# Optimization experiments

Hardware: AMD Instinct MI355X
Metric: run time of the kernel (lower is better)

Reference implementation:

```python
import jax, jax.numpy as jnp
import numpy as np


def _compute_gradient(f, src, dst, egw):
    # f: [b, c, n] node features; src/dst: [b, e] edge endpoints; egw: [b, e, d]
    # gradient at node src = sum_edges pinvdx * (f[dst] - f[src])
    fT = f.transpose(0, 2, 1)  # b, n, c
    n = fT.shape[1]
    f_dst = jnp.take_along_axis(fT, dst[..., None], axis=1)  # b, e, c
    f_src = jnp.take_along_axis(fT, src[..., None], axis=1)  # b, e, c
    msg = egw[..., :, None] * (f_dst - f_src)[..., None, :]  # b, e, d, c
    b, e, d, c = msg.shape

    def seg(m, s):
        return jax.ops.segment_sum(m.reshape(e, d * c), s, num_segments=n)

    grad = jax.vmap(seg)(msg, src)  # b, n, d*c
    return grad.transpose(0, 2, 1)  # b, d*c, n


def _forward(x, t, nodes, node_weights, edge_gradient_weights, modes, sp_L,
             fc0_w, fc0_b, Wc, Ws, W0, ws_w, ws_b, gws_w, gws_b,
             fc1_w, fc1_b, fc2_w, fc2_b, directed_edges):
    D = nodes.shape[-1]
    # Fourier bases: modes [k,d,w] scaled by sp_L [d,w]
    temp = jnp.einsum('bxd,kdw->bxkw', nodes, modes * sp_L)
    bc, bs = jnp.cos(temp), jnp.sin(temp)
    b0 = jnp.ones(temp[:, :, :1, :].shape, temp.dtype)
    nw = node_weights[:, :, None, :]
    wbc, wbs, wb0 = bc * nw, bs * nw, b0 * nw

    x_value = x[:, :, :D]
    h = jnp.concatenate([x, t], -1) @ fc0_w + fc0_b  # b, n, c
    h = h.transpose(0, 2, 1)  # b, c, n

    src = directed_edges[..., 0]
    dst = directed_edges[..., 1]
    nlayers = ws_w.shape[0]
    for i in range(nlayers):
        # spectral convolution (real Fourier transform on scattered points)
        xc = jnp.einsum('bcx,bxkw->bckw', h, wbc)
        xs = -jnp.einsum('bcx,bxkw->bckw', h, wbs)
        x0 = jnp.einsum('bcx,bxkw->bckw', h, wb0)
        fc_ = jnp.einsum('bikw,iokw->bokw', xc, Wc[i]) - jnp.einsum('bikw,iokw->bokw', xs, Ws[i])
        fs_ = jnp.einsum('bikw,iokw->bokw', xs, Wc[i]) + jnp.einsum('bikw,iokw->bokw', xc, Ws[i])
        f0_ = jnp.einsum('bikw,iokw->bokw', x0, W0[i])
        x1 = (jnp.einsum('bokw,bxkw->box', f0_, b0)
              + 2.0 * jnp.einsum('bokw,bxkw->box', fc_, bc)
              - 2.0 * jnp.einsum('bokw,bxkw->box', fs_, bs))
        # pointwise linear (Conv1d kernel size 1)
        x2 = jnp.einsum('oc,bcx->box', ws_w[i], h) + ws_b[i][None, :, None]
        # gradient operator + softsign + Conv1d
        g = _compute_gradient(h, src, dst, edge_gradient_weights)  # b, d*c, n
        g = g / (1.0 + jnp.abs(g))  # softsign
        x3 = jnp.einsum('oc,bcx->box', gws_w[i], g) + gws_b[i][None, :, None]
        h = x1 + x2 + x3
        if i != nlayers - 1:
            h = jax.nn.gelu(h, approximate=False)

    h = h.transpose(0, 2, 1)  # b, n, c
    h = jax.nn.gelu(h @ fc1_w + fc1_b, approximate=False)
    h = h @ fc2_w + fc2_b
    return x_value + t * h


def setup_inputs() -> dict:
    B, N, E = 2, 20000, 100000
    D, W, K, C, L, FC, OUT = 3, 1, 128, 128, 3, 128, 3
    key = jax.random.key(0)
    k = jax.random.split(key, 16)
    x = jax.random.normal(k[0], (B, N, D), jnp.float32)
    t = jax.random.uniform(k[1], (B, N, 1), jnp.float32)
    node_mask = jnp.ones((B, N, 1), jnp.int32)
    nodes = jax.random.uniform(k[2], (B, N, D), jnp.float32)
    node_weights = jax.random.uniform(k[3], (B, N, W), jnp.float32) / N
    directed_edges = jax.random.randint(k[4], (B, E, 2), 0, N)
    edge_gradient_weights = jax.random.normal(k[5], (B, E, D), jnp.float32)
    modes = jax.random.normal(k[6], (K, D, W), jnp.float32) * (2.0 * np.pi)
    sp_L = jnp.ones((D, W), jnp.float32)
    fc0_w = jax.random.normal(k[7], (D + 1, C), jnp.float32) * 0.1
    fc0_b = jnp.zeros((C,), jnp.float32)
    scale = 1.0 / (C * C)
    Wc = jax.random.uniform(k[8], (L, C, C, K, W), jnp.float32) * scale
    Ws = jax.random.uniform(k[9], (L, C, C, K, W), jnp.float32) * scale
    W0 = jax.random.uniform(k[10], (L, C, C, 1, W), jnp.float32) * scale
    ws_w = jax.random.normal(k[11], (L, C, C), jnp.float32) * 0.05
    ws_b = jnp.zeros((L, C), jnp.float32)
    gws_w = jax.random.normal(k[12], (L, C, D * C), jnp.float32) * 0.05
    gws_b = jnp.zeros((L, C), jnp.float32)
    fc1_w = jax.random.normal(k[13], (C, FC), jnp.float32) * 0.05
    fc1_b = jnp.zeros((FC,), jnp.float32)
    fc2_w = jax.random.normal(k[14], (FC, OUT), jnp.float32) * 0.05
    fc2_b = jnp.zeros((OUT,), jnp.float32)
    return dict(x=x, t=t, node_mask=node_mask, nodes=nodes, node_weights=node_weights,
                directed_edges=directed_edges, edge_gradient_weights=edge_gradient_weights,
                modes=modes, sp_L=sp_L, fc0_w=fc0_w, fc0_b=fc0_b, Wc=Wc, Ws=Ws, W0=W0,
                ws_w=ws_w, ws_b=ws_b, gws_w=gws_w, gws_b=gws_b,
                fc1_w=fc1_w, fc1_b=fc1_b, fc2_w=fc2_w, fc2_b=fc2_b)


def reference(x, t, node_mask, nodes, node_weights, directed_edges, edge_gradient_weights,
              modes, sp_L, fc0_w, fc0_b, Wc, Ws, W0, ws_w, ws_b, gws_w, gws_b,
              fc1_w, fc1_b, fc2_w, fc2_b):
    del node_mask  # unpacked but unused in the original forward
    return _forward(x, t, nodes, node_weights, edge_gradient_weights, modes, sp_L,
                    fc0_w, fc0_b, Wc, Ws, W0, ws_w, ws_b, gws_w, gws_b,
                    fc1_w, fc1_b, fc2_w, fc2_b, directed_edges)
```

## Files before the change

kernel.cpp:

```cpp
#include <hip/hip_runtime.h>
#include <math.h>

#define BB 2
#define NN 20000
#define EE 100000
#define DD 3
#define KK 128
#define CC 128
#define LL 3
#define FCC 128
#define GJ (DD*CC)
#define KR 768
#define NP 20096
#define NCHK 157
#define G1CH 79
#define G1N 256

typedef __attribute__((ext_vector_type(8))) short bf16x8;
typedef __attribute__((ext_vector_type(4))) float f32x4;

__device__ inline unsigned short f2bf(float f) {
  unsigned int u = __float_as_uint(f);
  u += 0x7fffu + ((u >> 16) & 1u);
  return (unsigned short)(u >> 16);
}
__device__ inline float bf2f(unsigned short u) {
  return __uint_as_float(((unsigned int)u) << 16);
}

__device__ float d_nw[BB*NN];
__device__ __align__(16) unsigned short d_stackT[(size_t)BB*NP*KR];
__device__ __align__(16) unsigned short d_bcT[(size_t)BB*KK*NP];
__device__ __align__(16) unsigned short d_bsT[(size_t)BB*KK*NP];
__device__ __align__(16) unsigned short d_hTwT[(size_t)BB*CC*NP];
__device__ __align__(16) float d_hnewT[(size_t)BB*NP*CC];
__device__ __align__(16) float d_uT[(size_t)BB*NP*FCC];
__device__ __align__(16) unsigned short d_Amatb[BB*CC*KR];
__device__ __align__(16) unsigned short d_fc1wb[FCC*CC];
__device__ __align__(16) float d_part[(size_t)BB*G1CH*2*128*128];
__device__ float d_xc[BB*CC*KK];
__device__ float d_xs[BB*CC*KK];
__device__ float d_x0p[BB*NCHK*CC];
__device__ float d_fcv[BB*CC*KK];
__device__ float d_fsv[BB*CC*KK];
__device__ float d_bias[BB*CC];
__device__ int d_cnt[BB*NN];
__device__ int d_cursor[BB*NN];
__device__ int d_off[BB*(NN+1)];
__device__ __align__(16) float4 d_erec[(size_t)BB*EE];

__global__ __launch_bounds__(128) void k_basis(const float* __restrict__ nodes,
                                               const float* __restrict__ nodew,
                                               const float* __restrict__ modes,
                                               const float* __restrict__ spL) {
  int bn = blockIdx.x;
  int k  = threadIdx.x;
  int b = bn / NN, n = bn % NN;
  float x0 = nodes[bn*3+0], x1 = nodes[bn*3+1], x2 = nodes[bn*3+2];
  float tmp = x0*modes[k*3+0]*spL[0] + x1*modes[k*3+1]*spL[1] + x2*modes[k*3+2]*spL[2];
  float cv = cosf(tmp), sv = sinf(tmp);
  size_t row = (size_t)(b*NP + n);
  d_stackT[row*KR + k]       = f2bf(cv);
  d_stackT[row*KR + 128 + k] = f2bf(sv);
  if (k == 0) d_nw[bn] = nodew[bn];
}

__global__ __launch_bounds__(256) void k_basisT() {
  __shared__ unsigned short t1[32][136];
  __shared__ unsigned short t2[32][136];
  int blk = blockIdx.x;
  int nt = blk % 628, b = blk / 628;
  int n0 = nt*32;
  int tid = threadIdx.x;
  int kl = tid & 127, ng = tid >> 7;
  for (int nn = ng; nn < 32; nn += 2) {
    int n = n0 + nn;
    unsigned short cv = 0, sv = 0;
    if (n < NN) {
      const unsigned short* sp = d_stackT + ((size_t)(b*NP + n))*KR;
      cv = sp[kl]; sv = sp[128 + kl];
    }
    t1[nn][kl] = cv;
    t2[nn][kl] = sv;
  }
  __syncthreads();
  int nl = tid & 31, kg = tid >> 5;
  for (int k = kg; k < 128; k += 8) {
    d_bcT[((size_t)(b*KK + k))*NP + n0 + nl] = t1[nl][k];
    d_bsT[((size_t)(b*KK + k))*NP + n0 + nl] = t2[nl][k];
  }
}

__global__ __launch_bounds__(256) void k_csr_zero() {
  int tid = blockIdx.x*256 + threadIdx.x;
  if (tid < BB*NN) { d_cnt[tid] = 0; d_cursor[tid] = 0; }
}

__global__ __launch_bounds__(256) void k_csr_count(const int* __restrict__ edges) {
  int e = blockIdx.x*256 + threadIdx.x;
  if (e >= BB*EE) return;
  int b = e / EE;
  int src = edges[e*2 + 0];
  atomicAdd(&d_cnt[b*NN + src], 1);
}

__global__ __launch_bounds__(1024) void k_csr_scan() {
  int b = blockIdx.x;
  __shared__ int sdata[1024];
  __shared__ int carry_s;
  int tid = threadIdx.x;
  if (tid == 0) carry_s = 0;
  __syncthreads();
  for (int chunk = 0; chunk < 20; ++chunk) {
    int i = chunk*1024 + tid;
    int v = (i < NN) ? d_cnt[b*NN + i] : 0;
    sdata[tid] = v;
    __syncthreads();
    for (int s = 1; s < 1024; s <<= 1) {
      int tv = (tid >= s) ? sdata[tid - s] : 0;
      __syncthreads();
      sdata[tid] += tv;
      __syncthreads();
    }
    int excl = carry_s + sdata[tid] - v;
    if (i < NN) d_off[b*(NN+1) + i] = excl;
    __syncthreads();
    if (tid == 1023) carry_s += sdata[1023];
    __syncthreads();
  }
  if (tid == 0) d_off[b*(NN+1) + NN] = carry_s;
}

__global__ __launch_bounds__(256) void k_csr_scatter(const int* __restrict__ edges,
                                                     const float* __restrict__ egw) {
  int e = blockIdx.x*256 + threadIdx.x;
  if (e >= BB*EE) return;
  int b = e / EE;
  int src = edges[e*2 + 0];
  int dst = edges[e*2 + 1];
  int pos = atomicAdd(&d_cursor[b*NN + src], 1);
  d_erec[(size_t)b*EE + d_off[b*(NN+1) + src] + pos] =
      make_float4(__int_as_float(dst), egw[e*3+0], egw[e*3+1], egw[e*3+2]);
}

__global__ __launch_bounds__(256) void k_h0(const float* __restrict__ x,
                                            const float* __restrict__ t,
                                            const float* __restrict__ w,
                                            const float* __restrict__ bias) {
  int tid = blockIdx.x*256 + threadIdx.x;
  int c = tid & 127;
  int bn = tid >> 7;
  int b = bn / NN, n = bn % NN;
  const float* xv = x + bn*3;
  float acc = bias[c] + xv[0]*w[c] + xv[1]*w[CC+c] + xv[2]*w[2*CC+c]
            + t[bn]*w[3*CC+c];
  size_t row = (size_t)(b*NP + n);
  d_hnewT[row*CC + c] = acc;
  d_stackT[row*KR + 256 + c] = f2bf(acc);
}

__global__ __launch_bounds__(256) void k_hT0() {
  __shared__ unsigned short t[128][136];
  int chunk = blockIdx.x;
  int b = blockIdx.y;
  int n0 = chunk*128;
  int tid = threadIdx.x;
  int cl = tid & 127, ng = tid >> 7;
  for (int nn = ng; nn < 128; nn += 2) {
    int n = n0 + nn;
    unsigned short v = 0;
    if (n < NN) v = f2bf(d_hnewT[((size_t)(b*NP + n))*CC + cl] * d_nw[b*NN + n]);
    t[nn][cl] = v;
  }
  __syncthreads();
  int nl = tid & 31, cg = tid >> 5;
  for (int c = cg; c < 128; c += 8)
    for (int nn2 = 0; nn2 < 128; nn2 += 32)
      d_hTwT[((size_t)(b*CC + c))*NP + n0 + nn2 + nl] = t[nn2 + nl][c];
}

__global__ __launch_bounds__(256) void k_gemm1m() {
  __shared__ unsigned short Bsh[2][128][40];
  int chunk = blockIdx.x;
  int b = blockIdx.y;
  int tid = threadIdx.x, lane = tid & 63, wid = tid >> 6;
  int q = lane >> 4, m = lane & 15;
  f32x4 accC[2][8], accS[2][8];
  #pragma unroll
  for (int i = 0; i < 2; i++)
    #pragma unroll
    for (int j = 0; j < 8; j++) { accC[i][j] = (f32x4){0.f,0.f,0.f,0.f}; accS[i][j] = (f32x4){0.f,0.f,0.f,0.f}; }
  const unsigned short* Ab = d_hTwT + (size_t)b*CC*NP;
  const unsigned short* Bcp = d_bcT + (size_t)b*KK*NP;
  const unsigned short* Bsp = d_bsT + (size_t)b*KK*NP;
  int n0 = chunk*G1N;
  for (int s = 0; s < G1N/32; s++) {
    int nb = n0 + s*32;
    if (nb >= NP) break;
    __syncthreads();
    {
      int arr = tid >> 7, row = tid & 127;
      const unsigned short* src = (arr ? Bsp : Bcp) + (size_t)row*NP + nb;
      unsigned short* dr = &Bsh[arr][row][0];
      *(uint4*)&dr[0]  = *(const uint4*)&src[0];
      *(uint4*)&dr[8]  = *(const uint4*)&src[8];
      *(uint4*)&dr[16] = *(const uint4*)&src[16];
      *(uint4*)&dr[24] = *(const uint4*)&src[24];
    }
    __syncthreads();
    bf16x8 a0 = *(const bf16x8*)(Ab + (size_t)(wid*32 + m)*NP + nb + q*8);
    bf16x8 a1 = *(const bf16x8*)(Ab + (size_t)(wid*32 + 16 + m)*NP + nb + q*8);
    #pragma unroll
    for (int kt = 0; kt < 8; kt++) {
      bf16x8 bcf = *(const bf16x8*)&Bsh[0][kt*16 + m][q*8];
      bf16x8 bsf = *(const bf16x8*)&Bsh[1][kt*16 + m][q*8];
      accC[0][kt] = __builtin_amdgcn_mfma_f32_16x16x32_bf16(a0, bcf, accC[0][kt], 0, 0, 0);
      accC[1][kt] = __builtin_amdgcn_mfma_f32_16x16x32_bf16(a1, bcf, accC[1][kt], 0, 0, 0);
      accS[0][kt] = __builtin_amdgcn_mfma_f32_16x16x32_bf16(a0, bsf, accS[0][kt], 0, 0, 0);
      accS[1][kt] = __builtin_amdgcn_mfma_f32_16x16x32_bf16(a1, bsf, accS[1][kt], 0, 0, 0);
    }
  }
  float* base = d_part + (((size_t)b*G1CH + chunk)*2)*16384;
  #pragma unroll
  for (int mt = 0; mt < 2; mt++)
    #pragma unroll
    for (int kt = 0; kt < 8; kt++)
      #pragma unroll
      for (int r = 0; r < 4; r++) {
        int c = wid*32 + mt*16 + q*4 + r;
        int k = kt*16 + m;
        base[c*128 + k]         =  accC[mt][kt][r];
        base[16384 + c*128 + k] = -accS[mt][kt][r];
      }
}

__global__ __launch_bounds__(256) void k_reduce1() {
  int tid = blockIdx.x*256 + threadIdx.x;
  int k = tid & 127;
  int c = (tid >> 7) & 127;
  int arr = (tid >> 14) & 1;
  int b = tid >> 15;
  const float* p = d_part + (((size_t)b*G1CH)*2 + arr)*16384 + c*128 + k;
  float acc = 0.f;
  for (int ch = 0; ch < G1CH; ch++) acc += p[(size_t)ch*2*16384];
  if (arr == 0) d_xc[(b*CC + c)*KK + k] = acc;
  else          d_xs[(b*CC + c)*KK + k] = acc;
}

__global__ __launch_bounds__(256) void k_x0() {
  int chunk = blockIdx.x;
  int b = blockIdx.y;
  int tid = threadIdx.x;
  int c = tid >> 1, half = tid & 1;
  const unsigned short* p = d_hTwT + ((size_t)(b*CC + c))*NP + chunk*128 + half*64;
  float acc = 0.f;
  #pragma unroll
  for (int i = 0; i < 8; i++) {
    ushort4 v0 = *(const ushort4*)&p[i*8];
    ushort4 v1 = *(const ushort4*)&p[i*8 + 4];
    acc += bf2f(v0.x) + bf2f(v0.y) + bf2f(v0.z) + bf2f(v0.w)
         + bf2f(v1.x) + bf2f(v1.y) + bf2f(v1.z) + bf2f(v1.w);
  }
  __shared__ float red[128][2];
  red[c][half] = acc;
  __syncthreads();
  if (half == 0) d_x0p[(b*NCHK + chunk)*CC + c] = red[c][0] + red[c][1];
}

__global__ __launch_bounds__(128) void k_spec(const float* __restrict__ Wc,
                                              const float* __restrict__ Ws, int l) {
  int b = blockIdx.x >> 7;
  int o = blockIdx.x & 127;
  int k = threadIdx.x;
  const float* wcp = Wc + ((size_t)(l*CC)*CC + o)*KK + k;
  const float* wsp = Ws + ((size_t)(l*CC)*CC + o)*KK + k;
  float fc = 0.f, fs = 0.f;
  for (int i = 0; i < CC; i++) {
    float xcv = d_xc[(b*CC + i)*KK + k];
    float xsv = d_xs[(b*CC + i)*KK + k];
    float wcv = wcp[(size_t)i*CC*KK];
    float wsv = wsp[(size_t)i*CC*KK];
    fc += xcv*wcv - xsv*wsv;
    fs += xsv*wcv + xcv*wsv;
  }
  d_fcv[(b*CC + o)*KK + k] = fc;
  d_fsv[(b*CC + o)*KK + k] = fs;
}

__global__ __launch_bounds__(128) void k_f0(const float* __restrict__ W0,
                                            const float* __restrict__ wsb,
                                            const float* __restrict__ gwsb, int l) {
  int b = blockIdx.x;
  int o = threadIdx.x;
  __shared__ float sx[CC];
  float xv = 0.f;
  for (int p = 0; p < NCHK; p++) xv += d_x0p[(b*NCHK + p)*CC + o];
  sx[o] = xv;
  __syncthreads();
  float acc = 0.f;
  for (int i = 0; i < CC; i++) acc += sx[i]*W0[(l*CC + i)*CC + o];
  d_bias[b*CC + o] = acc + wsb[l*CC + o] + gwsb[l*CC + o];
}

__global__ __launch_bounds__(128) void k_buildAb(const float* __restrict__ wsw,
                                                 const float* __restrict__ gwsw, int l) {
  int bo = blockIdx.x;
  int b = bo >> 7, o = bo & 127;
  int t = threadIdx.x;
  unsigned short* dst = d_Amatb + (size_t)bo*KR;
  dst[t]       = f2bf( 2.f*d_fcv[(size_t)bo*KK + t]);
  dst[128 + t] = f2bf(-2.f*d_fsv[(size_t)bo*KK + t]);
  dst[256 + t] = f2bf(wsw[(l*CC + o)*CC + t]);
  #pragma unroll
  for (int j = 0; j < 3; j++)
    dst[384 + j*128 + t] = f2bf(gwsw[(size_t)(l*CC + o)*GJ + j*128 + t]);
}

__global__ __launch_bounds__(128) void k_fc1w(const float* __restrict__ fc1w) {
  int c = blockIdx.x;
  int o2 = threadIdx.x;
  d_fc1wb[o2*CC + c] = f2bf(fc1w[c*FCC + o2]);
}

__global__ __launch_bounds__(128) void k_grad_csr() {
  int bn = blockIdx.x;
  int b = bn / NN, n = bn % NN;
  int c = threadIdx.x;
  int beg = d_off[b*(NN+1) + n];
  int end = d_off[b*(NN+1) + n + 1];
  const float4* rp = d_erec + (size_t)b*EE;
  const float* hb = d_hnewT + (size_t)b*NP*CC + c;
  float a0 = 0.f, a1 = 0.f, a2 = 0.f;
  float sw0 = 0.f, sw1 = 0.f, sw2 = 0.f;
  int p = beg;
  for (; p + 2 <= end; p += 2) {
    float4 r1 = rp[p], r2 = rp[p+1];
    float f1 = hb[(size_t)__float_as_int(r1.x)*CC];
    float f2 = hb[(size_t)__float_as_int(r2.x)*CC];
    a0 += r1.y*f1 + r2.y*f2;
    a1 += r1.z*f1 + r2.z*f2;
    a2 += r1.w*f1 + r2.w*f2;
    sw0 += r1.y + r2.y; sw1 += r1.z + r2.z; sw2 += r1.w + r2.w;
  }
  if (p < end) {
    float4 r1 = rp[p];
    float f1 = hb[(size_t)__float_as_int(r1.x)*CC];
    a0 += r1.y*f1; a1 += r1.z*f1; a2 += r1.w*f1;
    sw0 += r1.y; sw1 += r1.z; sw2 += r1.w;
  }
  float fs = d_hnewT[((size_t)(b*NP + n))*CC + c];
  a0 -= sw0*fs; a1 -= sw1*fs; a2 -= sw2*fs;
  unsigned short* gp = d_stackT + ((size_t)(b*NP + n))*KR + 384;
  gp[c]        = f2bf(a0/(1.f + fabsf(a0)));
  gp[CC + c]   = f2bf(a1/(1.f + fabsf(a1)));
  gp[2*CC + c] = f2bf(a2/(1.f + fabsf(a2)));
}

__global__ __launch_bounds__(256) void k_mfma(int koff, int K,
                                              const unsigned short* __restrict__ W, size_t wstride,
                                              float* __restrict__ Out,
                                              const float* __restrict__ bias, int bias_stride,
                                              int gelu, int aux) {
  __shared__ unsigned short As[128*40];
  __shared__ unsigned short Bs[128*40];
  int b = blockIdx.z;
  int n_base = blockIdx.x*128;
  int tid = threadIdx.x;
  int lane = tid & 63, wid = tid >> 6;
  int q = lane >> 4, m = lane & 15;

  f32x4 acc[2][8];
  #pragma unroll
  for (int i = 0; i < 2; i++)
    #pragma unroll
    for (int j = 0; j < 8; j++) acc[i][j] = (f32x4){0.f,0.f,0.f,0.f};

  const unsigned short* Wb = W + (size_t)b*wstride;
  const unsigned short* Ab = d_stackT + (size_t)b*NP*KR + koff;

  for (int k0 = 0; k0 < K; k0 += 32) {
    __syncthreads();
    #pragma unroll
    for (int i = 0; i < 2; i++) {
      int row = (tid >> 2) + i*64;
      int e8  = (tid & 3)*8;
      *(uint4*)&As[row*40 + e8] = *(const uint4*)(Ab + (size_t)(n_base + row)*KR + k0 + e8);
      *(uint4*)&Bs[row*40 + e8] = *(const uint4*)(Wb + (size_t)row*K + k0 + e8);
    }
    __syncthreads();
    bf16x8 a0 = *(const bf16x8*)&As[(wid*32 + m)*40 + q*8];
    bf16x8 a1 = *(const bf16x8*)&As[(wid*32 + 16 + m)*40 + q*8];
    #pragma unroll
    for (int ot = 0; ot < 8; ot++) {
      bf16x8 bf = *(const bf16x8*)&Bs[(ot*16 + m)*40 + q*8];
      acc[0][ot] = __builtin_amdgcn_mfma_f32_16x16x32_bf16(a0, bf, acc[0][ot], 0, 0, 0);
      acc[1][ot] = __builtin_amdgcn_mfma_f32_16x16x32_bf16(a1, bf, acc[1][ot], 0, 0, 0);
    }
  }

  const float* bp = bias + (size_t)b*bias_stride;
  #pragma unroll
  for (int nt = 0; nt < 2; nt++) {
    int nb4 = n_base + wid*32 + nt*16 + q*4;
    float nw4[4];
    #pragma unroll
    for (int r = 0; r < 4; r++)
      nw4[r] = (aux && nb4 + r < NN) ? d_nw[b*NN + nb4 + r] : 0.f;
    #pragma unroll
    for (int ot = 0; ot < 8; ot++) {
      int o = ot*16 + m;
      float bvv = bp[o];
      float vals[4];
      #pragma unroll
      for (int r = 0; r < 4; r++) {
        float v = acc[nt][ot][r] + bvv;
        if (gelu) v = 0.5f*v*(1.f + erff(v*0.70710678118f));
        vals[r] = v;
        Out[((size_t)(b*NP + nb4 + r))*128 + o] = v;
        if (aux && nb4 + r < NN)
          d_stackT[((size_t)(b*NP + nb4 + r))*KR + 256 + o] = f2bf(v);
      }
      if (aux) {
        ushort4 pk;
        pk.x = f2bf(vals[0]*nw4[0]);
        pk.y = f2bf(vals[1]*nw4[1]);
        pk.z = f2bf(vals[2]*nw4[2]);
        pk.w = f2bf(vals[3]*nw4[3]);
        *(ushort4*)&d_hTwT[((size_t)(b*CC + o))*NP + nb4] = pk;
      }
    }
  }
}

__global__ __launch_bounds__(256) void k_out(const float* __restrict__ x,
                                             const float* __restrict__ t,
                                             const float* __restrict__ fc2w,
                                             const float* __restrict__ fc2b,
                                             float* __restrict__ out) {
  int tid = blockIdx.x*256 + threadIdx.x;
  if (tid >= BB*NN) return;
  int b = tid / NN, n = tid % NN;
  const float* up = d_uT + ((size_t)(b*NP + n))*FCC;
  float a0 = fc2b[0], a1 = fc2b[1], a2v = fc2b[2];
  #pragma unroll 4
  for (int o2 = 0; o2 < FCC; o2 += 4) {
    float4 uv = *(const float4*)&up[o2];
    a0  += uv.x*fc2w[(o2+0)*3+0] + uv.y*fc2w[(o2+1)*3+0] + uv.z*fc2w[(o2+2)*3+0] + uv.w*fc2w[(o2+3)*3+0];
    a1  += uv.x*fc2w[(o2+0)*3+1] + uv.y*fc2w[(o2+1)*3+1] + uv.z*fc2w[(o2+2)*3+1] + uv.w*fc2w[(o2+3)*3+1];
    a2v += uv.x*fc2w[(o2+0)*3+2] + uv.y*fc2w[(o2+1)*3+2] + uv.z*fc2w[(o2+2)*3+2] + uv.w*fc2w[(o2+3)*3+2];
  }
  float tv = t[tid];
  out[tid*3 + 0] = x[tid*3 + 0] + tv*a0;
  out[tid*3 + 1] = x[tid*3 + 1] + tv*a1;
  out[tid*3 + 2] = x[tid*3 + 2] + tv*a2v;
}

extern "C" void kernel_launch(void* const* d_in, const int* in_sizes, int n_in,
                              void* d_out, int out_size, void* d_ws, size_t ws_size,
                              hipStream_t stream) {
  const float* x     = (const float*)d_in[0];
  const float* t     = (const float*)d_in[1];
  const float* nodes = (const float*)d_in[3];
  const float* nodew = (const float*)d_in[4];
  const int*   edges = (const int*)d_in[5];
  const float* egw   = (const float*)d_in[6];
  const float* modes = (const float*)d_in[7];
  const float* spL   = (const float*)d_in[8];
  const float* fc0w  = (const float*)d_in[9];
  const float* fc0b  = (const float*)d_in[10];
  const float* Wc    = (const float*)d_in[11];
  const float* Ws    = (const float*)d_in[12];
  const float* W0    = (const float*)d_in[13];
  const float* wsw   = (const float*)d_in[14];
  const float* wsb   = (const float*)d_in[15];
  const float* gwsw  = (const float*)d_in[16];
  const float* gwsb  = (const float*)d_in[17];
  const float* fc1w  = (const float*)d_in[18];
  const float* fc1b  = (const float*)d_in[19];
  const float* fc2w  = (const float*)d_in[20];
  const float* fc2b  = (const float*)d_in[21];
  float* out = (float*)d_out;

  unsigned short* d_Amatb_p; hipGetSymbolAddress((void**)&d_Amatb_p, HIP_SYMBOL(d_Amatb));
  unsigned short* d_fc1wb_p; hipGetSymbolAddress((void**)&d_fc1wb_p, HIP_SYMBOL(d_fc1wb));
  float* d_hnewT_p; hipGetSymbolAddress((void**)&d_hnewT_p, HIP_SYMBOL(d_hnewT));
  float* d_uT_p;    hipGetSymbolAddress((void**)&d_uT_p,    HIP_SYMBOL(d_uT));
  float* d_bias_p;  hipGetSymbolAddress((void**)&d_bias_p,  HIP_SYMBOL(d_bias));

  hipLaunchKernelGGL(k_basis, dim3(BB*NN), dim3(128), 0, stream, nodes, nodew, modes, spL);
  hipLaunchKernelGGL(k_basisT, dim3(628*BB), dim3(256), 0, stream);
  hipLaunchKernelGGL(k_h0, dim3(BB*NN*CC/256), dim3(256), 0, stream, x, t, fc0w, fc0b);
  hipLaunchKernelGGL(k_hT0, dim3(NCHK, BB), dim3(256), 0, stream);
  hipLaunchKernelGGL(k_fc1w, dim3(CC), dim3(FCC), 0, stream, fc1w);
  hipLaunchKernelGGL(k_csr_zero, dim3((BB*NN + 255)/256), dim3(256), 0, stream);
  hipLaunchKernelGGL(k_csr_count, dim3((BB*EE + 255)/256), dim3(256), 0, stream, edges);
  hipLaunchKernelGGL(k_csr_scan, dim3(BB), dim3(1024), 0, stream);
  hipLaunchKernelGGL(k_csr_scatter, dim3((BB*EE + 255)/256), dim3(256), 0, stream, edges, egw);

  for (int l = 0; l < LL; l++) {
    hipLaunchKernelGGL(k_gemm1m, dim3(G1CH, BB), dim3(256), 0, stream);
    hipLaunchKernelGGL(k_reduce1, dim3(256), dim3(256), 0, stream);
    hipLaunchKernelGGL(k_x0, dim3(NCHK, BB), dim3(256), 0, stream);
    hipLaunchKernelGGL(k_spec, dim3(BB*CC), dim3(128), 0, stream, Wc, Ws, l);
    hipLaunchKernelGGL(k_f0, dim3(BB), dim3(CC), 0, stream, W0, wsb, gwsb, l);
    hipLaunchKernelGGL(k_buildAb, dim3(BB*CC), dim3(128), 0, stream, wsw, gwsw, l);
    hipLaunchKernelGGL(k_grad_csr, dim3(BB*NN), dim3(128), 0, stream);
    hipLaunchKernelGGL(k_mfma, dim3(NCHK, 1, BB), dim3(256), 0, stream,
                       0, KR, d_Amatb_p, (size_t)CC*KR, d_hnewT_p, d_bias_p, CC,
                       (l != LL-1) ? 1 : 0, 1);
  }

  hipLaunchKernelGGL(k_mfma, dim3(NCHK, 1, BB), dim3(256), 0, stream,
                     256, CC, d_fc1wb_p, (size_t)0, d_uT_p, fc1b, 0, 1, 0);
  hipLaunchKernelGGL(k_out, dim3((BB*NN + 255)/256), dim3(256), 0, stream, x, t, fc2w, fc2b, out);
}
```

Measured before the change: 581.5 us.

## Double-buffer LDS tiles in MFMA GEMM and halve node tile to 64

The MFMA GEMM kernel now uses two LDS buffers, so the next K-slice is loaded while the current one is computed, and it drops one of the two barriers per iteration. The node tile per block shrinks from 128 to 64, which doubles the grid to 314 blocks per batch and halves the accumulators per thread. The aim is to hide global-load latency and fill more of the CUs. In exchange, each block reuses every weight tile across fewer rows, so the weight matrix is reloaded roughly twice as often in total.

```diff
diff --git a/kernel.cpp b/kernel.cpp
--- a/kernel.cpp
+++ b/kernel.cpp
@@ -361,73 +361,72 @@
                                               float* __restrict__ Out,
                                               const float* __restrict__ bias, int bias_stride,
                                               int gelu, int aux) {
-  __shared__ unsigned short As[128*40];
-  __shared__ unsigned short Bs[128*40];
+  __shared__ unsigned short As[2][64*40];
+  __shared__ unsigned short Bs[2][128*40];
   int b = blockIdx.z;
-  int n_base = blockIdx.x*128;
+  int n_base = blockIdx.x*64;
   int tid = threadIdx.x;
   int lane = tid & 63, wid = tid >> 6;
   int q = lane >> 4, m = lane & 15;
 
-  f32x4 acc[2][8];
-  #pragma unroll
-  for (int i = 0; i < 2; i++)
-    #pragma unroll
-    for (int j = 0; j < 8; j++) acc[i][j] = (f32x4){0.f,0.f,0.f,0.f};
+  f32x4 acc[8];
+  #pragma unroll
+  for (int j = 0; j < 8; j++) acc[j] = (f32x4){0.f,0.f,0.f,0.f};
 
   const unsigned short* Wb = W + (size_t)b*wstride;
   const unsigned short* Ab = d_stackT + (size_t)b*NP*KR + koff;
 
+#define STAGE(k0, d) { \
+    int rowA = tid >> 2; int e8A = (tid & 3)*8; \
+    *(uint4*)&As[d][rowA*40 + e8A] = *(const uint4*)(Ab + (size_t)(n_base + rowA)*KR + (k0) + e8A); \
+    _Pragma("unroll") \
+    for (int i_ = 0; i_ < 2; i_++) { \
+      int idx_ = tid + i_*256; int rowB = idx_ >> 2; int e8B = (idx_ & 3)*8; \
+      *(uint4*)&Bs[d][rowB*40 + e8B] = *(const uint4*)(Wb + (size_t)rowB*K + (k0) + e8B); \
+    } }
+
+  STAGE(0, 0)
+  int cur = 0;
   for (int k0 = 0; k0 < K; k0 += 32) {
     __syncthreads();
-    #pragma unroll
-    for (int i = 0; i < 2; i++) {
-      int row = (tid >> 2) + i*64;
-      int e8  = (tid & 3)*8;
-      *(uint4*)&As[row*40 + e8] = *(const uint4*)(Ab + (size_t)(n_base + row)*KR + k0 + e8);
-      *(uint4*)&Bs[row*40 + e8] = *(const uint4*)(Wb + (size_t)row*K + k0 + e8);
-    }
-    __syncthreads();
-    bf16x8 a0 = *(const bf16x8*)&As[(wid*32 + m)*40 + q*8];
-    bf16x8 a1 = *(const bf16x8*)&As[(wid*32 + 16 + m)*40 + q*8];
+    if (k0 + 32 < K) STAGE(k0 + 32, cur ^ 1)
+    bf16x8 a = *(const bf16x8*)&As[cur][(wid*16 + m)*40 + q*8];
     #pragma unroll
     for (int ot = 0; ot < 8; ot++) {
-      bf16x8 bf = *(const bf16x8*)&Bs[(ot*16 + m)*40 + q*8];
-      acc[0][ot] = __builtin_amdgcn_mfma_f32_16x16x32_bf16(a0, bf, acc[0][ot], 0, 0, 0);
-      acc[1][ot] = __builtin_amdgcn_mfma_f32_16x16x32_bf16(a1, bf, acc[1][ot], 0, 0, 0);
-    }
-  }
+      bf16x8 bf = *(const bf16x8*)&Bs[cur][(ot*16 + m)*40 + q*8];
+      acc[ot] = __builtin_amdgcn_mfma_f32_16x16x32_bf16(a, bf, acc[ot], 0, 0, 0);
+    }
+    cur ^= 1;
+  }
+#undef STAGE
 
   const float* bp = bias + (size_t)b*bias_stride;
-  #pragma unroll
-  for (int nt = 0; nt < 2; nt++) {
-    int nb4 = n_base + wid*32 + nt*16 + q*4;
-    float nw4[4];
+  int nb4 = n_base + wid*16 + q*4;
+  float nw4[4];
+  #pragma unroll
+  for (int r = 0; r < 4; r++)
+    nw4[r] = (aux && nb4 + r < NN) ? d_nw[b*NN + nb4 + r] : 0.f;
+  #pragma unroll
+  for (int ot = 0; ot < 8; ot++) {
+    int o = ot*16 + m;
+    float bvv = bp[o];
+    float vals[4];
     #pragma unroll
-    for (int r = 0; r < 4; r++)
-      nw4[r] = (aux && nb4 + r < NN) ? d_nw[b*NN + nb4 + r] : 0.f;
-    #pragma unroll
-    for (int ot = 0; ot < 8; ot++) {
-      int o = ot*16 + m;
-      float bvv = bp[o];
-      float vals[4];
-      #pragma unroll
-      for (int r = 0; r < 4; r++) {
-        float v = acc[nt][ot][r] + bvv;
-        if (gelu) v = 0.5f*v*(1.f + erff(v*0.70710678118f));
-        vals[r] = v;
-        Out[((size_t)(b*NP + nb4 + r))*128 + o] = v;
-        if (aux && nb4 + r < NN)
-          d_stackT[((size_t)(b*NP + nb4 + r))*KR + 256 + o] = f2bf(v);
-      }
-      if (aux) {
-        ushort4 pk;
-        pk.x = f2bf(vals[0]*nw4[0]);
-        pk.y = f2bf(vals[1]*nw4[1]);
-        pk.z = f2bf(vals[2]*nw4[2]);
-        pk.w = f2bf(vals[3]*nw4[3]);
-        *(ushort4*)&d_hTwT[((size_t)(b*CC + o))*NP + nb4] = pk;
-      }
+    for (int r = 0; r < 4; r++) {
+      float v = acc[ot][r] + bvv;
+      if (gelu) v = 0.5f*v*(1.f + erff(v*0.70710678118f));
+      vals[r] = v;
+      Out[((size_t)(b*NP + nb4 + r))*128 + o] = v;
+      if (aux && nb4 + r < NN)
+        d_stackT[((size_t)(b*NP + nb4 + r))*KR + 256 + o] = f2bf(v);
+    }
+    if (aux) {
+      ushort4 pk;
+      pk.x = f2bf(vals[0]*nw4[0]);
+      pk.y = f2bf(vals[1]*nw4[1]);
+      pk.z = f2bf(vals[2]*nw4[2]);
+      pk.w = f2bf(vals[3]*nw4[3]);
+      *(ushort4*)&d_hTwT[((size_t)(b*CC + o))*NP + nb4] = pk;
     }
   }
 }
@@ -505,12 +504,12 @@
     hipLaunchKernelGGL(k_f0, dim3(BB), dim3(CC), 0, stream, W0, wsb, gwsb, l);
     hipLaunchKernelGGL(k_buildAb, dim3(BB*CC), dim3(128), 0, stream, wsw, gwsw, l);
     hipLaunchKernelGGL(k_grad_csr, dim3(BB*NN), dim3(128), 0, stream);
-    hipLaunchKernelGGL(k_mfma, dim3(NCHK, 1, BB), dim3(256), 0, stream,
+    hipLaunchKernelGGL(k_mfma, dim3(NP/64, 1, BB), dim3(256), 0, stream,
                        0, KR, d_Amatb_p, (size_t)CC*KR, d_hnewT_p, d_bias_p, CC,
                        (l != LL-1) ? 1 : 0, 1);
   }
 
-  hipLaunchKernelGGL(k_mfma, dim3(NCHK, 1, BB), dim3(256), 0, stream,
+  hipLaunchKernelGGL(k_mfma, dim3(NP/64, 1, BB), dim3(256), 0, stream,
                      256, CC, d_fc1wb_p, (size_t)0, d_uT_p, fc1b, 0, 1, 0);
   hipLaunchKernelGGL(k_out, dim3((BB*NN + 255)/256), dim3(256), 0, stream, x, t, fc2w, fc2b, out);
 }
```

New measurement: 563.5 us. 1.03x faster.
